# Performance work log

Measured on AMD Instinct MI355X. Metric: run time of the kernel, lower is better.

Reference implementation:

```python
import jax, jax.numpy as jnp
import numpy as np

SUBSTEPS = 2  # fixed RK4 substeps per save interval (replaces adaptive diffrax solver)


def setup_inputs() -> dict:
    key = jax.random.key(0)
    k = jax.random.split(key, 6)
    dim, hidden, neighbors, T = 512, 2048, 512, 9
    ts = jnp.linspace(0.0, 1.0, T, dtype=jnp.float32)
    y0 = jax.random.normal(k[0], (dim,), dtype=jnp.float32)
    Dy0 = jax.random.normal(k[1], (neighbors, dim), dtype=jnp.float32) * 0.01
    W1 = jax.random.normal(k[2], (dim, hidden), dtype=jnp.float32) / np.sqrt(dim).astype(np.float32)
    b1 = jax.random.normal(k[3], (hidden,), dtype=jnp.float32) * 0.01
    W2 = jax.random.normal(k[4], (hidden, dim), dtype=jnp.float32) / np.sqrt(hidden).astype(np.float32)
    b2 = jax.random.normal(k[5], (dim,), dtype=jnp.float32) * 0.01
    return {"ts": ts, "y0": y0, "Dy0": Dy0, "W1": W1, "b1": b1, "W2": W2, "b2": b2}


def reference(ts, y0, Dy0, W1, b1, W2, b2):
    tmap = jax.tree_util.tree_map

    def f(y):  # autonomous NeuralODE vector field: 2-layer tanh MLP
        return jnp.tanh(y @ W1 + b1) @ W2 + b2

    def rhs(u):
        y, Dy = u                      # y: [dim], Dy: [neighbors, dim]
        z = y + Dy                     # [neighbors, dim]

        def second_order(z_):          # per-neighbor, z_: [dim]
            def first_order(y_):
                return jax.jvp(f, (y_,), (z_ - y_,))
            (dy, dDy1), (_, dDy2) = jax.jvp(first_order, (y,), (z_ - y,))
            return dy, 1.5 * dDy1 + 0.5 * dDy2

        dy, dDy = jax.vmap(second_order, out_axes=(None, 0))(z)
        return (dy, dDy)

    def axpy(u, k, c):
        return tmap(lambda a, b: a + c * b, u, k)

    def rk4(u, dt):
        k1 = rhs(u)
        k2 = rhs(axpy(u, k1, dt * 0.5))
        k3 = rhs(axpy(u, k2, dt * 0.5))
        k4 = rhs(axpy(u, k3, dt))
        return tmap(lambda a, a1, a2, a3, a4: a + (dt / 6.0) * (a1 + 2.0 * a2 + 2.0 * a3 + a4),
                    u, k1, k2, k3, k4)

    def interval(u, tpair):
        t0, t1 = tpair
        dt = (t1 - t0) / SUBSTEPS
        def body(u_, _):
            return rk4(u_, dt), None
        u_new, _ = jax.lax.scan(body, u, None, length=SUBSTEPS)
        return u_new, u_new

    u0 = (y0, Dy0)
    _, (ys, Dys) = jax.lax.scan(interval, u0, (ts[:-1], ts[1:]))
    ys = jnp.concatenate([y0[None], ys], axis=0)        # [T, dim]
    Dys = jnp.concatenate([Dy0[None], Dys], axis=0)     # [T, neighbors, dim]
    # pack (y, Dy) trajectories into one array: [T, 1+neighbors, dim]
    return jnp.concatenate([ys[:, None, :], Dys], axis=1)
```

## Files before the change

kernel.cpp:

```cpp
#include <hip/hip_runtime.h>
#include <hip/hip_bf16.h>

typedef __attribute__((ext_vector_type(8))) short short8;
typedef float f32x4 __attribute__((ext_vector_type(4)));

#define DIM 512
#define HID 2048
#define ROWSZ (513*512)
#define DT 0.0625f

#define WAITV(n) asm volatile("s_waitcnt vmcnt(" #n ")" ::: "memory")
#define WAITL()  asm volatile("s_waitcnt lgkmcnt(0)" ::: "memory")
#define SBAR()   asm volatile("s_barrier" ::: "memory")
typedef const __attribute__((address_space(1))) void* gas1;
typedef __attribute__((address_space(3))) void* las3;
#define GLL16(g,l,aux) __builtin_amdgcn_global_load_lds((gas1)(g),(las3)(l),16,0,aux)
#define GLL4(g,l,aux)  __builtin_amdgcn_global_load_lds((gas1)(g),(las3)(l),4,0,aux)

__device__ __forceinline__ unsigned short f2bfu(float f){ __hip_bfloat16 h=__float2bfloat16(f); return *(unsigned short*)&h; }

__device__ __forceinline__ void xbar(int* arr, int* gen, int target, bool lead){
  asm volatile("s_waitcnt vmcnt(0) lgkmcnt(0)" ::: "memory");
  __syncthreads();
  if (threadIdx.x == 0){
    __hip_atomic_fetch_add(arr, 1, __ATOMIC_RELAXED, __HIP_MEMORY_SCOPE_AGENT);
    if (lead){
      while (__hip_atomic_load(arr, __ATOMIC_RELAXED, __HIP_MEMORY_SCOPE_AGENT) < 32*target)
        __builtin_amdgcn_s_sleep(2);
      __hip_atomic_store(gen, target, __ATOMIC_RELAXED, __HIP_MEMORY_SCOPE_AGENT);
    } else {
      while (__hip_atomic_load(gen, __ATOMIC_RELAXED, __HIP_MEMORY_SCOPE_AGENT) < target)
        __builtin_amdgcn_s_sleep(4);
    }
  }
  __syncthreads();
}

__device__ __forceinline__ void post_flag(int* f, int seq){
  asm volatile("s_waitcnt vmcnt(0) lgkmcnt(0)" ::: "memory");
  __syncthreads();
  if (threadIdx.x == 0)
    __hip_atomic_store(f, seq, __ATOMIC_RELAXED, __HIP_MEMORY_SCOPE_AGENT);
}
__device__ __forceinline__ void wait_flags32(int* base, int seq){
  if (threadIdx.x < 32){
    while (__hip_atomic_load(&base[threadIdx.x], __ATOMIC_RELAXED, __HIP_MEMORY_SCOPE_AGENT) < seq)
      __builtin_amdgcn_s_sleep(2);
  }
  __syncthreads();
}
__device__ __forceinline__ void wait_flags16(int* base, int seq){
  if (threadIdx.x < 16){
    while (__hip_atomic_load(&base[threadIdx.x], __ATOMIC_RELAXED, __HIP_MEMORY_SCOPE_AGENT) < seq)
      __builtin_amdgcn_s_sleep(2);
  }
  __syncthreads();
}

__global__ void k_transpose_bf16(const float* __restrict__ src,
                                 __hip_bfloat16* __restrict__ dst, int R, int C) {
  __shared__ float tile[32][33];
  int c0 = blockIdx.x * 32, r0 = blockIdx.y * 32;
  int tx = threadIdx.x & 31, ty = threadIdx.x >> 5;
  for (int i = 0; i < 32; i += 8)
    tile[ty + i][tx] = src[(size_t)(r0 + ty + i) * C + c0 + tx];
  __syncthreads();
  for (int i = 0; i < 32; i += 8)
    dst[(size_t)(c0 + ty + i) * R + r0 + tx] = __float2bfloat16(tile[tx][ty + i]);
}

__global__ __launch_bounds__(512, 1) void k_persist(
    const float* __restrict__ y0, const float* __restrict__ Dy0,
    const unsigned short* __restrict__ W1t, const unsigned short* __restrict__ W2t,
    const float* __restrict__ b1, const float* __restrict__ b2,
    unsigned short* __restrict__ Vbuf, unsigned short* __restrict__ tbuf,
    float* __restrict__ yts, unsigned short* __restrict__ a_ss, float* __restrict__ pbuf,
    int* __restrict__ ctrl, float* __restrict__ out) {
  __shared__ __align__(16) short W1L[64 * 512];
  __shared__ __align__(16) short W2L[32 * 1024];
  __shared__ __align__(16) short ring[3][4096];
  __shared__ float ytL[DIM];
  __shared__ __align__(16) unsigned short ytB[DIM];
  __shared__ __align__(16) unsigned short asL[1024];
  __shared__ float pacc[64];
  __shared__ float c1L[64], c2L[64];
  __shared__ int bcast[2];

  const int t = threadIdx.x;
  if (t == 0) {
    int x;
    asm volatile("s_getreg_b32 %0, hwreg(HW_REG_XCC_ID)" : "=s"(x));
    x &= 7;
    bcast[0] = x;
    bcast[1] = atomicAdd(&ctrl[x], 1);
  }
  __syncthreads();
  const int xcd = bcast[0];
  const int sl  = bcast[1] & 31;
  const bool lead = (sl == 0);
  int* arr = ctrl + 64 + xcd * 64;
  int* gen = arr + 32;
  int* flgAb = ctrl + 704 + xcd * 32;
  int* flgBb = ctrl + 960 + xcd * 32;

  const int w = t >> 6, lane = t & 63, quad = lane >> 4, l16 = lane & 15;
  const int r8 = lane >> 3;
  const int mX = xcd * 64;
  const int nA = sl * 64;
  const int ni = sl >> 1, kq = sl & 1;
  const int nB = ni * 32;
  const int kb = kq * 1024;
  float* ytx = yts + xcd * DIM;
  unsigned short* asx = a_ss + xcd * HID;
  float* rec = pbuf + (size_t)(xcd * 16 + ni) * 2112;
  int* flg = ctrl + 576 + xcd * 16 + ni;

  const int awm = (w & 1) * 32, awn = (w >> 1) * 16;
  const int bwm = (w >> 1) * 16, bwn = (w & 1) * 16;

  const short8 z8 = {0,0,0,0,0,0,0,0};

  f32x4 DyR = {0.f,0.f,0.f,0.f}, K1 = DyR, K2 = DyR, K3 = DyR;
  float yR = 0.f, kd1 = 0.f, kd2 = 0.f, kd3 = 0.f;
  const int erow0 = mX + bwm + quad * 4;
  const int ecol  = nB + bwn + l16;

  auto issueA = [&](int buf, int c) {
    int k0 = c * 64;
    GLL16(Vbuf + (size_t)(mX + w * 8 + r8) * DIM + k0 + (((lane & 7) ^ r8) << 3),
          &ring[buf][(w * 8) * 64], 1);
  };
  auto issueB = [&](int buf, int c) {
    int k0 = kb + c * 64;
    GLL16(tbuf + (size_t)(mX + w * 8 + r8) * HID + k0 + (((lane & 7) ^ r8) << 3),
          &ring[buf][(w * 8) * 64], 1);
  };

#pragma unroll
  for (int i = 0; i < 8; ++i) {
    int r = w * 8 + i;
    int src = ((lane & ~7) | ((lane & 7) ^ (r & 7))) << 3;
    GLL16(W1t + (size_t)(nA + r) * DIM + src, &W1L[r * 512], 0);
  }
#pragma unroll
  for (int i = 0; i < 4; ++i) {
    int r = w * 4 + i;
#pragma unroll
    for (int h2 = 0; h2 < 2; ++h2) {
      int g0 = h2 * 64 + lane;
      int src = ((g0 & ~7) | ((g0 & 7) ^ (r & 7))) << 3;
      GLL16(W2t + (size_t)(nB + r) * HID + kb + src, &W2L[r * 1024 + h2 * 512], 0);
    }
  }
  if (kq == 0) {
#pragma unroll
    for (int r = 0; r < 4; ++r) {
      float v = Dy0[(size_t)(erow0 + r) * DIM + ecol];
      DyR[r] = v;
      Vbuf[(size_t)(erow0 + r) * DIM + ecol] = f2bfu(v);
      out[DIM + (size_t)(erow0 + r) * DIM + ecol] = v;
    }
    if (t < 32) {
      float v = y0[nB + t];
      yR = v;
      ytx[nB + t] = v;
      if (xcd == 0) out[nB + t] = v;
    }
  }
  WAITV(0);
  __syncthreads();
  xbar(arr, gen, 1, lead);

  for (int ss = 0; ss < 16; ++ss) {
    for (int st = 0; st < 4; ++st) {
      const float cn = (st == 2) ? DT : 0.5f * DT;
      const int seq = ss * 4 + st + 1;
      {
        wait_flags32(flgBb, seq - 1);
        GLL4(ytx + w * 64 + lane, &ytL[w * 64], 1);
        issueA(0, 0); issueA(1, 1);
        WAITV(2); SBAR();
        ytB[t] = f2bfu(ytL[t]);
        f32x4 acc0 = {0.f,0.f,0.f,0.f}, acc1 = acc0, acc2 = acc0;
        short8 ra0[2][2], ra1[2][2], rb[2][2], ya[2][2];
        const int pa0 = awm + l16, pa1 = awm + 16 + l16, pbW = awn + l16;
        WAITV(1); WAITL(); SBAR();
        {
          const short* tA = ring[0];
#pragma unroll
          for (int k2 = 0; k2 < 2; ++k2) {
            int lg = k2 * 4 + quad;
            ra0[0][k2] = *(const short8*)&tA[pa0 * 64 + ((lg ^ (pa0 & 7)) << 3)];
            ra1[0][k2] = *(const short8*)&tA[pa1 * 64 + ((lg ^ (pa1 & 7)) << 3)];
            int gb = lg;
            rb[0][k2] = *(const short8*)&W1L[pbW * 512 + (((gb & ~7) | ((gb & 7) ^ (pbW & 7))) << 3)];
            short8 yv = *(const short8*)&ytB[gb * 8];
            if (l16 != 0) yv = z8;
            ya[0][k2] = yv;
          }
        }
        WAITL();
#pragma unroll
        for (int c = 0; c < 8; ++c) {
          const int pr = c & 1, nx = pr ^ 1;
          if (c < 6)       { issueA((c + 2) % 3, c + 2); WAITV(1); }
          else if (c == 6) { WAITV(0); }
          if (c < 7) {
            SBAR();
            const short* tA = ring[(c + 1) % 3];
#pragma unroll
            for (int k2 = 0; k2 < 2; ++k2) {
              int lg = k2 * 4 + quad;
              ra0[nx][k2] = *(const short8*)&tA[pa0 * 64 + ((lg ^ (pa0 & 7)) << 3)];
              ra1[nx][k2] = *(const short8*)&tA[pa1 * 64 + ((lg ^ (pa1 & 7)) << 3)];
              int gb = (c + 1) * 8 + lg;
              rb[nx][k2] = *(const short8*)&W1L[pbW * 512 + (((gb & ~7) | ((gb & 7) ^ (pbW & 7))) << 3)];
              short8 yv = *(const short8*)&ytB[gb * 8];
              if (l16 != 0) yv = z8;
              ya[nx][k2] = yv;
            }
          }
#pragma unroll
          for (int k2 = 0; k2 < 2; ++k2) {
            acc0 = __builtin_amdgcn_mfma_f32_16x16x32_bf16(ra0[pr][k2], rb[pr][k2], acc0, 0, 0, 0);
            acc1 = __builtin_amdgcn_mfma_f32_16x16x32_bf16(ra1[pr][k2], rb[pr][k2], acc1, 0, 0, 0);
            acc2 = __builtin_amdgcn_mfma_f32_16x16x32_bf16(ya[pr][k2],  rb[pr][k2], acc2, 0, 0, 0);
          }
          if (c < 7) WAITL();
        }
        if ((w & 1) == 0 && quad == 0) pacc[awn + l16] = acc2[0];
        WAITL(); SBAR();
        if (t < 64) {
          float hsum = b1[nA + t] + pacc[t];
          float a = tanhf(hsum);
          float ap = 1.f - a * a;
          c1L[t] = ap; c2L[t] = -a * ap;
          asx[nA + t] = f2bfu(a);
        }
        WAITL(); SBAR();
        int row0 = mX + awm + quad * 4;
        int coln = nA + awn + l16;
        float C1 = c1L[awn + l16], C2 = c2L[awn + l16];
#pragma unroll
        for (int r = 0; r < 4; ++r) {
          float g0 = acc0[r], g1 = acc1[r];
          tbuf[(size_t)(row0 + r) * HID + coln]      = f2bfu(g0 * (C1 + C2 * g0));
          tbuf[(size_t)(row0 + 16 + r) * HID + coln] = f2bfu(g1 * (C1 + C2 * g1));
        }
        post_flag(&flgAb[sl], seq);
      }
      {
        wait_flags16(flgAb + kq * 16, seq);
        GLL4((const unsigned short*)asx + kb + w * 128 + lane * 2, &asL[w * 128], 1);
        issueB(0, 0); issueB(1, 1);
        WAITV(2); SBAR();
        f32x4 acc = {0.f,0.f,0.f,0.f}, acc2 = acc;
        short8 rba[2][2], rbw[2][2], aa[2][2];
        const int paB = bwm + l16, pbB = bwn + l16;
        WAITV(1); SBAR();
        {
          const short* tA = ring[0];
#pragma unroll
          for (int k2 = 0; k2 < 2; ++k2) {
            int lg = k2 * 4 + quad;
            rba[0][k2] = *(const short8*)&tA[paB * 64 + ((lg ^ (paB & 7)) << 3)];
            int gb = lg;
            rbw[0][k2] = *(const short8*)&W2L[pbB * 1024 + (((gb & ~7) | ((gb & 7) ^ (pbB & 7))) << 3)];
            short8 av = *(const short8*)&asL[gb * 8];
            if (l16 != 0) av = z8;
            aa[0][k2] = av;
          }
        }
        WAITL();
#pragma unroll
        for (int c = 0; c < 16; ++c) {
          const int pr = c & 1, nx = pr ^ 1;
          if (c < 14)       { issueB((c + 2) % 3, c + 2); WAITV(1); }
          else if (c == 14) { WAITV(0); }
          if (c < 15) {
            SBAR();
            const short* tA = ring[(c + 1) % 3];
#pragma unroll
            for (int k2 = 0; k2 < 2; ++k2) {
              int lg = k2 * 4 + quad;
              rba[nx][k2] = *(const short8*)&tA[paB * 64 + ((lg ^ (paB & 7)) << 3)];
              int gb = (c + 1) * 8 + lg;
              rbw[nx][k2] = *(const short8*)&W2L[pbB * 1024 + (((gb & ~7) | ((gb & 7) ^ (pbB & 7))) << 3)];
              short8 av = *(const short8*)&asL[gb * 8];
              if (l16 != 0) av = z8;
              aa[nx][k2] = av;
            }
          }
#pragma unroll
          for (int k2 = 0; k2 < 2; ++k2) {
            acc  = __builtin_amdgcn_mfma_f32_16x16x32_bf16(rba[pr][k2], rbw[pr][k2], acc, 0, 0, 0);
            acc2 = __builtin_amdgcn_mfma_f32_16x16x32_bf16(aa[pr][k2],  rbw[pr][k2], acc2, 0, 0, 0);
          }
          if (c < 15) WAITL();
        }
        if (w < 2 && quad == 0) pacc[bwn + l16] = acc2[0];
        WAITL(); SBAR();
        if (kq == 1) {
          int lrow = bwm + quad * 4, lcol = bwn + l16;
#pragma unroll
          for (int r = 0; r < 4; ++r) rec[(lrow + r) * 32 + lcol] = acc[r];
          if (t < 32) rec[2048 + t] = pacc[t];
          asm volatile("s_waitcnt vmcnt(0)" ::: "memory");
          __syncthreads();
          if (t == 0) {
            __hip_atomic_store(flg, seq, __ATOMIC_RELAXED, __HIP_MEMORY_SCOPE_AGENT);
            __hip_atomic_store(&flgBb[sl], seq, __ATOMIC_RELAXED, __HIP_MEMORY_SCOPE_AGENT);
          }
        } else {
          if (t == 0) {
            while (__hip_atomic_load(flg, __ATOMIC_RELAXED, __HIP_MEMORY_SCOPE_AGENT) < seq)
              __builtin_amdgcn_s_sleep(1);
          }
          __syncthreads();
          float* pLDS = (float*)&ring[0][0];
          GLL16(rec + w * 256 + lane * 4, pLDS + w * 256, 1);
          if (w == 0) GLL4(rec + 2048 + lane, pLDS + 2048, 1);
          WAITV(0);
          __syncthreads();
          int lrow = bwm + quad * 4, lcol = bwn + l16;
          f32x4 o = acc;
#pragma unroll
          for (int r = 0; r < 4; ++r) o[r] += pLDS[(lrow + r) * 32 + lcol];
          if (st == 0) K1 = o; else if (st == 1) K2 = o; else if (st == 2) K3 = o;
          if (st < 3) {
#pragma unroll
            for (int r = 0; r < 4; ++r) {
              float v = DyR[r] + cn * o[r];
              Vbuf[(size_t)(erow0 + r) * DIM + ecol] = f2bfu(v);
            }
          } else {
            const float dt6 = DT / 6.f;
#pragma unroll
            for (int r = 0; r < 4; ++r) {
              float v = DyR[r] + dt6 * (K1[r] + 2.f * K2[r] + 2.f * K3[r] + o[r]);
              DyR[r] = v;
              Vbuf[(size_t)(erow0 + r) * DIM + ecol] = f2bfu(v);
              if (ss & 1) out[(size_t)(ss / 2 + 1) * ROWSZ + DIM + (size_t)(erow0 + r) * DIM + ecol] = v;
            }
          }
          if (t < 32) {
            float k4 = pacc[t] + pLDS[2048 + t] + b2[nB + t];
            if (st == 0) kd1 = k4; else if (st == 1) kd2 = k4; else if (st == 2) kd3 = k4;
            if (st < 3) {
              ytx[nB + t] = yR + cn * k4;
            } else {
              yR += (DT / 6.f) * (kd1 + 2.f * kd2 + 2.f * kd3 + k4);
              ytx[nB + t] = yR;
              if ((ss & 1) && xcd == 0) out[(size_t)(ss / 2 + 1) * ROWSZ + nB + t] = yR;
            }
          }
          post_flag(&flgBb[sl], seq);
        }
      }
    }
  }
}

extern "C" void kernel_launch(void* const* d_in, const int* in_sizes, int n_in,
                              void* d_out, int out_size, void* d_ws, size_t ws_size,
                              hipStream_t stream) {
  const float* y0  = (const float*)d_in[1];
  const float* Dy0 = (const float*)d_in[2];
  const float* W1  = (const float*)d_in[3];
  const float* b1  = (const float*)d_in[4];
  const float* W2  = (const float*)d_in[5];
  const float* b2  = (const float*)d_in[6];
  float* out = (float*)d_out;

  char* p = (char*)d_ws;
  auto alloc = [&](size_t bytes) {
    char* r = p;
    p += (bytes + 255) & ~(size_t)255;
    return r;
  };
  unsigned short* W1t  = (unsigned short*)alloc((size_t)HID * DIM * 2);
  unsigned short* W2t  = (unsigned short*)alloc((size_t)DIM * HID * 2);
  unsigned short* Vbuf = (unsigned short*)alloc((size_t)DIM * DIM * 2);
  unsigned short* tbuf = (unsigned short*)alloc((size_t)DIM * HID * 2);
  float* yts  = (float*)alloc(8 * DIM * 4);
  unsigned short* a_ss = (unsigned short*)alloc(8 * HID * 2);
  float* pbuf = (float*)alloc((size_t)8 * 16 * 2112 * 4);
  int* ctrl   = (int*)alloc(8192);

  hipMemsetAsync(ctrl, 0, 8192, stream);
  k_transpose_bf16<<<dim3(HID / 32, DIM / 32), 256, 0, stream>>>(W1, (__hip_bfloat16*)W1t, DIM, HID);
  k_transpose_bf16<<<dim3(DIM / 32, HID / 32), 256, 0, stream>>>(W2, (__hip_bfloat16*)W2t, HID, DIM);
  k_persist<<<256, 512, 0, stream>>>(y0, Dy0, W1t, W2t, b1, b2,
                                     Vbuf, tbuf, yts, a_ss, pbuf, ctrl, out);
}
```

Measured before the change: 795.0 us.

## Give each block full-K slice in stage B, dropping cross-block partial-sum exchange

```diff
diff --git a/kernel.cpp b/kernel.cpp
--- a/kernel.cpp
+++ b/kernel.cpp
@@ -49,13 +49,6 @@
   }
   __syncthreads();
 }
-__device__ __forceinline__ void wait_flags16(int* base, int seq){
-  if (threadIdx.x < 16){
-    while (__hip_atomic_load(&base[threadIdx.x], __ATOMIC_RELAXED, __HIP_MEMORY_SCOPE_AGENT) < seq)
-      __builtin_amdgcn_s_sleep(2);
-  }
-  __syncthreads();
-}
 
 __global__ void k_transpose_bf16(const float* __restrict__ src,
                                  __hip_bfloat16* __restrict__ dst, int R, int C) {
@@ -77,11 +70,11 @@
     float* __restrict__ yts, unsigned short* __restrict__ a_ss, float* __restrict__ pbuf,
     int* __restrict__ ctrl, float* __restrict__ out) {
   __shared__ __align__(16) short W1L[64 * 512];
-  __shared__ __align__(16) short W2L[32 * 1024];
+  __shared__ __align__(16) short W2L[16 * 2048];
   __shared__ __align__(16) short ring[3][4096];
   __shared__ float ytL[DIM];
   __shared__ __align__(16) unsigned short ytB[DIM];
-  __shared__ __align__(16) unsigned short asL[1024];
+  __shared__ __align__(16) unsigned short asL[2048];
   __shared__ float pacc[64];
   __shared__ float c1L[64], c2L[64];
   __shared__ int bcast[2];
@@ -107,23 +100,19 @@
   const int r8 = lane >> 3;
   const int mX = xcd * 64;
   const int nA = sl * 64;
-  const int ni = sl >> 1, kq = sl & 1;
-  const int nB = ni * 32;
-  const int kb = kq * 1024;
+  const int nB2 = sl * 16;
   float* ytx = yts + xcd * DIM;
   unsigned short* asx = a_ss + xcd * HID;
-  float* rec = pbuf + (size_t)(xcd * 16 + ni) * 2112;
-  int* flg = ctrl + 576 + xcd * 16 + ni;
 
   const int awm = (w & 1) * 32, awn = (w >> 1) * 16;
-  const int bwm = (w >> 1) * 16, bwn = (w & 1) * 16;
+  const int pj = w >> 1, ph = w & 1;
 
   const short8 z8 = {0,0,0,0,0,0,0,0};
 
   f32x4 DyR = {0.f,0.f,0.f,0.f}, K1 = DyR, K2 = DyR, K3 = DyR;
   float yR = 0.f, kd1 = 0.f, kd2 = 0.f, kd3 = 0.f;
-  const int erow0 = mX + bwm + quad * 4;
-  const int ecol  = nB + bwn + l16;
+  const int erow0 = mX + pj * 16 + quad * 4;
+  const int ecol  = nB2 + l16;
 
   auto issueA = [&](int buf, int c) {
     int k0 = c * 64;
@@ -131,7 +120,7 @@
           &ring[buf][(w * 8) * 64], 1);
   };
   auto issueB = [&](int buf, int c) {
-    int k0 = kb + c * 64;
+    int k0 = c * 64;
     GLL16(tbuf + (size_t)(mX + w * 8 + r8) * HID + k0 + (((lane & 7) ^ r8) << 3),
           &ring[buf][(w * 8) * 64], 1);
   };
@@ -143,16 +132,16 @@
     GLL16(W1t + (size_t)(nA + r) * DIM + src, &W1L[r * 512], 0);
   }
 #pragma unroll
-  for (int i = 0; i < 4; ++i) {
-    int r = w * 4 + i;
-#pragma unroll
-    for (int h2 = 0; h2 < 2; ++h2) {
-      int g0 = h2 * 64 + lane;
+  for (int i = 0; i < 2; ++i) {
+    int r = w * 2 + i;
+#pragma unroll
+    for (int j = 0; j < 4; ++j) {
+      int g0 = j * 64 + lane;
       int src = ((g0 & ~7) | ((g0 & 7) ^ (r & 7))) << 3;
-      GLL16(W2t + (size_t)(nB + r) * HID + kb + src, &W2L[r * 1024 + h2 * 512], 0);
+      GLL16(W2t + (size_t)(nB2 + r) * HID + src, &W2L[r * 2048 + j * 512], 0);
     }
   }
-  if (kq == 0) {
+  if (!ph) {
 #pragma unroll
     for (int r = 0; r < 4; ++r) {
       float v = Dy0[(size_t)(erow0 + r) * DIM + ecol];
@@ -160,12 +149,12 @@
       Vbuf[(size_t)(erow0 + r) * DIM + ecol] = f2bfu(v);
       out[DIM + (size_t)(erow0 + r) * DIM + ecol] = v;
     }
-    if (t < 32) {
-      float v = y0[nB + t];
-      yR = v;
-      ytx[nB + t] = v;
-      if (xcd == 0) out[nB + t] = v;
-    }
+  }
+  if (t < 16) {
+    float v = y0[nB2 + t];
+    yR = v;
+    ytx[nB2 + t] = v;
+    if (xcd == 0) out[nB2 + t] = v;
   }
   WAITV(0);
   __syncthreads();
@@ -250,82 +239,39 @@
         post_flag(&flgAb[sl], seq);
       }
       {
-        wait_flags16(flgAb + kq * 16, seq);
-        GLL4((const unsigned short*)asx + kb + w * 128 + lane * 2, &asL[w * 128], 1);
+        wait_flags32(flgAb, seq);
+        GLL4((const unsigned short*)asx + w * 128 + lane * 2, &asL[w * 128], 1);
+        GLL4((const unsigned short*)asx + 1024 + w * 128 + lane * 2, &asL[1024 + w * 128], 1);
         issueB(0, 0); issueB(1, 1);
         WAITV(2); SBAR();
         f32x4 acc = {0.f,0.f,0.f,0.f}, acc2 = acc;
-        short8 rba[2][2], rbw[2][2], aa[2][2];
-        const int paB = bwm + l16, pbB = bwn + l16;
-        WAITV(1); SBAR();
-        {
-          const short* tA = ring[0];
-#pragma unroll
-          for (int k2 = 0; k2 < 2; ++k2) {
-            int lg = k2 * 4 + quad;
-            rba[0][k2] = *(const short8*)&tA[paB * 64 + ((lg ^ (paB & 7)) << 3)];
-            int gb = lg;
-            rbw[0][k2] = *(const short8*)&W2L[pbB * 1024 + (((gb & ~7) | ((gb & 7) ^ (pbB & 7))) << 3)];
-            short8 av = *(const short8*)&asL[gb * 8];
-            if (l16 != 0) av = z8;
-            aa[0][k2] = av;
-          }
-        }
-        WAITL();
-#pragma unroll
-        for (int c = 0; c < 16; ++c) {
-          const int pr = c & 1, nx = pr ^ 1;
-          if (c < 14)       { issueB((c + 2) % 3, c + 2); WAITV(1); }
-          else if (c == 14) { WAITV(0); }
-          if (c < 15) {
-            SBAR();
-            const short* tA = ring[(c + 1) % 3];
-#pragma unroll
-            for (int k2 = 0; k2 < 2; ++k2) {
-              int lg = k2 * 4 + quad;
-              rba[nx][k2] = *(const short8*)&tA[paB * 64 + ((lg ^ (paB & 7)) << 3)];
-              int gb = (c + 1) * 8 + lg;
-              rbw[nx][k2] = *(const short8*)&W2L[pbB * 1024 + (((gb & ~7) | ((gb & 7) ^ (pbB & 7))) << 3)];
-              short8 av = *(const short8*)&asL[gb * 8];
-              if (l16 != 0) av = z8;
-              aa[nx][k2] = av;
-            }
-          }
-#pragma unroll
-          for (int k2 = 0; k2 < 2; ++k2) {
-            acc  = __builtin_amdgcn_mfma_f32_16x16x32_bf16(rba[pr][k2], rbw[pr][k2], acc, 0, 0, 0);
-            acc2 = __builtin_amdgcn_mfma_f32_16x16x32_bf16(aa[pr][k2],  rbw[pr][k2], acc2, 0, 0, 0);
-          }
-          if (c < 15) WAITL();
-        }
-        if (w < 2 && quad == 0) pacc[bwn + l16] = acc2[0];
+        const int paB = pj * 16 + l16;
+        const int lgW = ph * 4 + quad;
+#pragma unroll
+        for (int c = 0; c < 32; ++c) {
+          if (c < 31) { WAITV(1); } else { WAITV(0); }
+          SBAR();
+          if (c < 30) issueB((c + 2) % 3, c + 2);
+          const short* tA = ring[c % 3];
+          short8 a = *(const short8*)&tA[paB * 64 + ((lgW ^ (paB & 7)) << 3)];
+          int gb = c * 8 + lgW;
+          short8 b = *(const short8*)&W2L[l16 * 2048 + (((gb & ~7) | ((gb & 7) ^ (l16 & 7))) << 3)];
+          short8 av = *(const short8*)&asL[gb * 8];
+          if (l16 != 0) av = z8;
+          acc  = __builtin_amdgcn_mfma_f32_16x16x32_bf16(a,  b, acc,  0, 0, 0);
+          acc2 = __builtin_amdgcn_mfma_f32_16x16x32_bf16(av, b, acc2, 0, 0, 0);
+        }
+        float* red = (float*)&ring[0][0];
+        if (ph) {
+#pragma unroll
+          for (int r = 0; r < 4; ++r) red[pj * 256 + (quad * 4 + r) * 16 + l16] = acc[r];
+          if (w == 1 && quad == 0) red[1024 + l16] = acc2[0];
+        }
         WAITL(); SBAR();
-        if (kq == 1) {
-          int lrow = bwm + quad * 4, lcol = bwn + l16;
-#pragma unroll
-          for (int r = 0; r < 4; ++r) rec[(lrow + r) * 32 + lcol] = acc[r];
-          if (t < 32) rec[2048 + t] = pacc[t];
-          asm volatile("s_waitcnt vmcnt(0)" ::: "memory");
-          __syncthreads();
-          if (t == 0) {
-            __hip_atomic_store(flg, seq, __ATOMIC_RELAXED, __HIP_MEMORY_SCOPE_AGENT);
-            __hip_atomic_store(&flgBb[sl], seq, __ATOMIC_RELAXED, __HIP_MEMORY_SCOPE_AGENT);
-          }
-        } else {
-          if (t == 0) {
-            while (__hip_atomic_load(flg, __ATOMIC_RELAXED, __HIP_MEMORY_SCOPE_AGENT) < seq)
-              __builtin_amdgcn_s_sleep(1);
-          }
-          __syncthreads();
-          float* pLDS = (float*)&ring[0][0];
-          GLL16(rec + w * 256 + lane * 4, pLDS + w * 256, 1);
-          if (w == 0) GLL4(rec + 2048 + lane, pLDS + 2048, 1);
-          WAITV(0);
-          __syncthreads();
-          int lrow = bwm + quad * 4, lcol = bwn + l16;
-          f32x4 o = acc;
-#pragma unroll
-          for (int r = 0; r < 4; ++r) o[r] += pLDS[(lrow + r) * 32 + lcol];
+        if (!ph) {
+          f32x4 o;
+#pragma unroll
+          for (int r = 0; r < 4; ++r) o[r] = acc[r] + red[pj * 256 + (quad * 4 + r) * 16 + l16];
           if (st == 0) K1 = o; else if (st == 1) K2 = o; else if (st == 2) K3 = o;
           if (st < 3) {
 #pragma unroll
@@ -343,19 +289,19 @@
               if (ss & 1) out[(size_t)(ss / 2 + 1) * ROWSZ + DIM + (size_t)(erow0 + r) * DIM + ecol] = v;
             }
           }
-          if (t < 32) {
-            float k4 = pacc[t] + pLDS[2048 + t] + b2[nB + t];
-            if (st == 0) kd1 = k4; else if (st == 1) kd2 = k4; else if (st == 2) kd3 = k4;
-            if (st < 3) {
-              ytx[nB + t] = yR + cn * k4;
-            } else {
-              yR += (DT / 6.f) * (kd1 + 2.f * kd2 + 2.f * kd3 + k4);
-              ytx[nB + t] = yR;
-              if ((ss & 1) && xcd == 0) out[(size_t)(ss / 2 + 1) * ROWSZ + nB + t] = yR;
-            }
-          }
-          post_flag(&flgBb[sl], seq);
-        }
+        }
+        if (t < 16) {
+          float k4 = acc2[0] + red[1024 + t] + b2[nB2 + t];
+          if (st == 0) kd1 = k4; else if (st == 1) kd2 = k4; else if (st == 2) kd3 = k4;
+          if (st < 3) {
+            ytx[nB2 + t] = yR + cn * k4;
+          } else {
+            yR += (DT / 6.f) * (kd1 + 2.f * kd2 + 2.f * kd3 + k4);
+            ytx[nB2 + t] = yR;
+            if ((ss & 1) && xcd == 0) out[(size_t)(ss / 2 + 1) * ROWSZ + nB2 + t] = yR;
+          }
+        }
+        post_flag(&flgBb[sl], seq);
       }
     }
   }
```

Result: faster. 731.9 us (median of 2 runs) (-7.9%).
